# Optimization experiments

Hardware: AMD Instinct MI355X
Metric: run time of the kernel (lower is better)

## Reference

```python
import jax, jax.numpy as jnp
import numpy as np

N = 2048  # number of graph nodes


def setup_inputs() -> dict:
    key = jax.random.key(0)
    k1, k2, k3, k4 = jax.random.split(key, 4)
    # dense non-negative adjacency / association matrix
    A = jax.random.uniform(k1, (N, N), dtype=jnp.float32)
    # GTConv weights: layer0.conv1, layer0.conv2, layer1.conv1 (each (2,1,1,1))
    w1a = jax.random.normal(k2, (2, 1, 1, 1), dtype=jnp.float32)
    w1b = jax.random.normal(k3, (2, 1, 1, 1), dtype=jnp.float32)
    w2a = jax.random.normal(k4, (2, 1, 1, 1), dtype=jnp.float32)
    return {"A": A, "w1a": w1a, "w1b": w1b, "w2a": w2a}


def _gtconv(A4, w):
    # A4: (1,1,n,n); w: (2,1,1,1). softmax over dim=1 (singleton -> ones),
    # broadcast-multiply -> (2,1,n,n), sum over dim 0 -> (1,n,n)
    sw = jax.nn.softmax(w, axis=1)
    return jnp.sum(A4 * sw, axis=0)


def _norm(H):
    # H: (n,n). H <- diag(deg)^-1 @ (H + I), expressed as a row-scale
    # (identical math to the diagonal mm in the original).
    n = H.shape[0]
    H = H + jnp.eye(n, dtype=H.dtype)
    deg = jnp.sum(H, axis=1)
    deg = jnp.where(deg <= 1e-10, jnp.ones_like(deg), deg)
    return H / deg[:, None]


def reference(A, w1a, w1b, w2a):
    A4 = A[None, None]  # (1,1,n,n) after the forward's unsqueeze + broadcast
    # layer 0 (first=True)
    a = _gtconv(A4, w1a)            # (1,n,n)
    b = _gtconv(A4, w1b)            # (1,n,n)
    H = jnp.matmul(a, b)            # (1,n,n)
    # layer 1 (first=False): normalization of H[0], then bmm with conv(A)
    H_ = _norm(H[0])[None]          # (1,n,n)
    a2 = _gtconv(A4, w2a)           # (1,n,n)
    H2 = jnp.matmul(H_, a2)         # (1,n,n)
    return H2
```

## Files before the change

### kernel.cpp

```cpp
#include <hip/hip_runtime.h>
#include <stdint.h>

#define N 2048
#define TILE 128
#define BK 64
#define KH 16
#define LDSW 72
#define RSTR 17
#define NN ((size_t)N * (size_t)N)

typedef unsigned short u16;
typedef __bf16 bf16x8 __attribute__((ext_vector_type(8)));
typedef unsigned short ushortx8 __attribute__((ext_vector_type(8)));
typedef float floatx4 __attribute__((ext_vector_type(4)));

static __device__ __forceinline__ u16 f2bf(float f) {
  unsigned int u = __builtin_bit_cast(unsigned int, f);
  return (u16)((u + 0x7fffu + ((u >> 16) & 1u)) >> 16);
}
static __device__ __forceinline__ float bf2f(u16 h) {
  unsigned int u = ((unsigned int)h) << 16;
  return __builtin_bit_cast(float, u);
}

__global__ void cast_tr(const float* __restrict__ A, u16* __restrict__ Ab,
                        u16* __restrict__ Abt) {
  __shared__ float tile[32][33];
  const int tx = threadIdx.x, ty = threadIdx.y;
  const int c = blockIdx.x * 32 + tx;
#pragma unroll
  for (int i = 0; i < 4; i++) {
    const int r = blockIdx.y * 32 + ty + i * 8;
    const float v = A[(size_t)r * N + c];
    Ab[(size_t)r * N + c] = f2bf(v);
    tile[ty + i * 8][tx] = v;
  }
  __syncthreads();
  const int r2 = blockIdx.y * 32 + tx;
#pragma unroll
  for (int i = 0; i < 4; i++) {
    const int c2 = blockIdx.x * 32 + ty + i * 8;
    Abt[(size_t)c2 * N + r2] = f2bf(tile[tx][ty + i * 8]);
  }
}

__device__ __forceinline__ void gemm_core(const u16* __restrict__ L,
                                          const u16* __restrict__ Rt,
                                          float res[4][4]) {
  __shared__ __align__(16) u16 As[2][2][TILE * LDSW];
  __shared__ __align__(16) u16 Bs[2][2][TILE * LDSW];

  const int t = threadIdx.x;
  const int h = t >> 9;
  const int tl = t & 511;
  const int row0 = blockIdx.y * TILE;
  const int col0 = blockIdx.x * TILE;

  const int srow = tl >> 2;
  const int sc = (tl & 3) * 16;
  const u16* gA = L + (size_t)(row0 + srow) * N + h * (KH * BK) + sc;
  const u16* gB = Rt + (size_t)(col0 + srow) * N + h * (KH * BK) + sc;
  const int woff = srow * LDSW + sc;

  const int lane = t & 63;
  const int w = t >> 6;
  const int sub = w & 7;
  const int wr = (sub >> 2) * 64;
  const int wc = (sub & 3) * 32;
  const int lr = lane & 15;
  const int q = lane >> 4;
  const int abase = (wr + lr) * LDSW + q * 8;
  const int bbase = (wc + lr) * LDSW + q * 8;

  floatx4 acc[4][2];
#pragma unroll
  for (int i = 0; i < 4; i++)
#pragma unroll
    for (int j = 0; j < 2; j++) acc[i][j] = (floatx4){0.f, 0.f, 0.f, 0.f};

  ushortx8 sA[2][2], sB[2][2];
  sA[0][0] = *(const ushortx8*)(gA);
  sA[0][1] = *(const ushortx8*)(gA + 8);
  sB[0][0] = *(const ushortx8*)(gB);
  sB[0][1] = *(const ushortx8*)(gB + 8);
  sA[1][0] = *(const ushortx8*)(gA + BK);
  sA[1][1] = *(const ushortx8*)(gA + BK + 8);
  sB[1][0] = *(const ushortx8*)(gB + BK);
  sB[1][1] = *(const ushortx8*)(gB + BK + 8);
  *(ushortx8*)&As[h][0][woff] = sA[0][0];
  *(ushortx8*)&As[h][0][woff + 8] = sA[0][1];
  *(ushortx8*)&Bs[h][0][woff] = sB[0][0];
  *(ushortx8*)&Bs[h][0][woff + 8] = sB[0][1];
  __syncthreads();

#define GSTEP(i, cur, nxt)                                                    \
  {                                                                           \
    if ((i) + 2 < KH) {                                                       \
      sA[cur][0] = *(const ushortx8*)(gA + ((i) + 2) * BK);                   \
      sA[cur][1] = *(const ushortx8*)(gA + ((i) + 2) * BK + 8);               \
      sB[cur][0] = *(const ushortx8*)(gB + ((i) + 2) * BK);                   \
      sB[cur][1] = *(const ushortx8*)(gB + ((i) + 2) * BK + 8);               \
    }                                                                         \
    _Pragma("unroll") for (int kk = 0; kk < 2; kk++) {                        \
      bf16x8 af[4], bfr[2];                                                   \
      _Pragma("unroll") for (int mt = 0; mt < 4; mt++) af[mt] =               \
          __builtin_bit_cast(bf16x8,                                          \
              *(const ushortx8*)&As[h][cur][abase + kk * 32 + mt * 16 * LDSW]); \
      _Pragma("unroll") for (int nt = 0; nt < 2; nt++) bfr[nt] =              \
          __builtin_bit_cast(bf16x8,                                          \
              *(const ushortx8*)&Bs[h][cur][bbase + kk * 32 + nt * 16 * LDSW]); \
      _Pragma("unroll") for (int mt = 0; mt < 4; mt++)                        \
          _Pragma("unroll") for (int nt = 0; nt < 2; nt++) acc[mt][nt] =      \
              __builtin_amdgcn_mfma_f32_16x16x32_bf16(af[mt], bfr[nt],        \
                                                      acc[mt][nt], 0, 0, 0);  \
    }                                                                         \
    if ((i) + 1 < KH) {                                                       \
      *(ushortx8*)&As[h][nxt][woff] = sA[nxt][0];                             \
      *(ushortx8*)&As[h][nxt][woff + 8] = sA[nxt][1];                         \
      *(ushortx8*)&Bs[h][nxt][woff] = sB[nxt][0];                             \
      *(ushortx8*)&Bs[h][nxt][woff + 8] = sB[nxt][1];                         \
    }                                                                         \
    __syncthreads();                                                          \
  }

  for (int io = 0; io < KH; io += 2) {
    GSTEP(io, 0, 1)
    GSTEP(io + 1, 1, 0)
  }
#undef GSTEP

  float* red = (float*)&As[0][0][0];
  const int oh = 1 - h;
  const int rship = (sub * 2 + oh) * (64 * RSTR);
  const int rkeep = (sub * 2 + h) * (64 * RSTR);
#pragma unroll
  for (int mt = 0; mt < 4; mt++)
#pragma unroll
    for (int r = 0; r < 4; r++) {
      const float vship = h ? acc[mt][0][r] : acc[mt][1][r];
      red[rship + (mt * 16 + q * 4 + r) * RSTR + lr] = vship;
    }
  __syncthreads();
#pragma unroll
  for (int mt = 0; mt < 4; mt++)
#pragma unroll
    for (int r = 0; r < 4; r++) {
      const float vkeep = h ? acc[mt][1][r] : acc[mt][0][r];
      res[mt][r] = vkeep + red[rkeep + (mt * 16 + q * 4 + r) * RSTR + lr];
    }
}

__global__ __launch_bounds__(1024, 4) void gemm_aa(const u16* __restrict__ Ab,
                                                   const u16* __restrict__ Abt,
                                                   u16* __restrict__ Mb) {
  float res[4][4];
  gemm_core(Ab, Abt, res);
  const int t = threadIdx.x;
  const int lane = t & 63, w = t >> 6;
  const int sub = w & 7, h = w >> 3;
  const int wr = (sub >> 2) * 64, wc = (sub & 3) * 32;
  const int lr = lane & 15, q = lane >> 4;
  const int row0 = blockIdx.y * TILE, col0 = blockIdx.x * TILE;
  const int cc = col0 + wc + h * 16 + lr;
#pragma unroll
  for (int mt = 0; mt < 4; mt++)
#pragma unroll
    for (int r = 0; r < 4; r++) {
      const int rr = row0 + wr + mt * 16 + q * 4 + r;
      Mb[(size_t)rr * N + cc] = f2bf(res[mt][r]);
    }
}

__global__ void rowsum_k(const u16* __restrict__ Mb, float* __restrict__ rdeg) {
  const int row = blockIdx.x;
  const int t = threadIdx.x;
  const ushortx8 v = *((const ushortx8*)(Mb + (size_t)row * N) + t);
  float s = 0.f;
#pragma unroll
  for (int j = 0; j < 8; j++) s += bf2f(v[j]);
#pragma unroll
  for (int off = 32; off > 0; off >>= 1) s += __shfl_down(s, off, 64);
  __shared__ float ws[4];
  if ((t & 63) == 0) ws[t >> 6] = s;
  __syncthreads();
  if (t == 0) {
    float d = 4.f * (ws[0] + ws[1] + ws[2] + ws[3]) + 1.f;
    if (d <= 1e-10f) d = 1.f;
    rdeg[row] = 1.f / d;
  }
}

__global__ __launch_bounds__(1024, 4) void gemm_ma(const u16* __restrict__ Mb,
                                                   const u16* __restrict__ Abt,
                                                   const float* __restrict__ A,
                                                   const float* __restrict__ rdeg,
                                                   float* __restrict__ out) {
  float res[4][4];
  gemm_core(Mb, Abt, res);
  const int t = threadIdx.x;
  const int lane = t & 63, w = t >> 6;
  const int sub = w & 7, h = w >> 3;
  const int wr = (sub >> 2) * 64, wc = (sub & 3) * 32;
  const int lr = lane & 15, q = lane >> 4;
  const int row0 = blockIdx.y * TILE, col0 = blockIdx.x * TILE;
  const int cc = col0 + wc + h * 16 + lr;
#pragma unroll
  for (int mt = 0; mt < 4; mt++)
#pragma unroll
    for (int r = 0; r < 4; r++) {
      const int rr = row0 + wr + mt * 16 + q * 4 + r;
      out[(size_t)rr * N + cc] =
          (8.f * res[mt][r] + 2.f * A[(size_t)rr * N + cc]) * rdeg[rr];
    }
}

extern "C" void kernel_launch(void* const* d_in, const int* in_sizes, int n_in,
                              void* d_out, int out_size, void* d_ws, size_t ws_size,
                              hipStream_t stream) {
  const float* A = (const float*)d_in[0];
  float* out = (float*)d_out;
  char* ws = (char*)d_ws;
  u16* Ab = (u16*)ws;
  u16* Abt = (u16*)(ws + NN * 2);
  u16* Mb = (u16*)(ws + NN * 4);
  float* rdeg = (float*)(ws + NN * 6);

  cast_tr<<<dim3(N / 32, N / 32), dim3(32, 8), 0, stream>>>(A, Ab, Abt);
  gemm_aa<<<dim3(N / TILE, N / TILE), 1024, 0, stream>>>(Ab, Abt, Mb);
  rowsum_k<<<N, 256, 0, stream>>>(Mb, rdeg);
  gemm_ma<<<dim3(N / TILE, N / TILE), 1024, 0, stream>>>(Mb, Abt, A, rdeg, out);
}
```

Before: 128.6 us.

## Fuse row-degree sum into first GEMM epilogue and enlarge per-warp tiles

Removes the separate rowsum kernel by having gemm_aa accumulate fp32 row sums with shuffles and atomicAdd into a zeroed buffer, which gemm_ma then converts to the reciprocal degree. The GEMM core moves from 1024 to 512 threads, with each warp computing a 64x64 sub-tile and staging loads with single-step register prefetch instead of two steps ahead. This saves a launch and a full read of M, but adds atomics and more registers per thread. It also reduces prefetch depth, and the row sums now come from fp32 values rather than rounded bf16.

```diff
diff --git a/kernel.cpp b/kernel.cpp
--- a/kernel.cpp
+++ b/kernel.cpp
@@ -6,7 +6,7 @@
 #define BK 64
 #define KH 16
 #define LDSW 72
-#define RSTR 17
+#define RSTR 33
 #define NN ((size_t)N * (size_t)N)
 
 typedef unsigned short u16;
@@ -18,15 +18,15 @@
   unsigned int u = __builtin_bit_cast(unsigned int, f);
   return (u16)((u + 0x7fffu + ((u >> 16) & 1u)) >> 16);
 }
-static __device__ __forceinline__ float bf2f(u16 h) {
-  unsigned int u = ((unsigned int)h) << 16;
-  return __builtin_bit_cast(float, u);
-}
 
 __global__ void cast_tr(const float* __restrict__ A, u16* __restrict__ Ab,
-                        u16* __restrict__ Abt) {
+                        u16* __restrict__ Abt, float* __restrict__ rsum) {
   __shared__ float tile[32][33];
   const int tx = threadIdx.x, ty = threadIdx.y;
+  if (blockIdx.x == 0 && blockIdx.y == 0) {
+    const int tid = ty * 32 + tx;
+    for (int k = tid; k < N; k += 256) rsum[k] = 0.f;
+  }
   const int c = blockIdx.x * 32 + tx;
 #pragma unroll
   for (int i = 0; i < 4; i++) {
@@ -46,79 +46,85 @@
 
 __device__ __forceinline__ void gemm_core(const u16* __restrict__ L,
                                           const u16* __restrict__ Rt,
-                                          float res[4][4]) {
+                                          float res[4][8]) {
   __shared__ __align__(16) u16 As[2][2][TILE * LDSW];
   __shared__ __align__(16) u16 Bs[2][2][TILE * LDSW];
 
   const int t = threadIdx.x;
-  const int h = t >> 9;
-  const int tl = t & 511;
+  const int h = t >> 8;
+  const int tl = t & 255;
   const int row0 = blockIdx.y * TILE;
   const int col0 = blockIdx.x * TILE;
 
-  const int srow = tl >> 2;
-  const int sc = (tl & 3) * 16;
-  const u16* gA = L + (size_t)(row0 + srow) * N + h * (KH * BK) + sc;
-  const u16* gB = Rt + (size_t)(col0 + srow) * N + h * (KH * BK) + sc;
-  const int woff = srow * LDSW + sc;
+  int goff[4], woff[4];
+#pragma unroll
+  for (int c = 0; c < 4; c++) {
+    const int rowc = c * 32 + (tl >> 3);
+    const int colc = (tl & 7) * 8;
+    goff[c] = rowc * N + colc;
+    woff[c] = rowc * LDSW + colc;
+  }
+  const u16* gA = L + (size_t)row0 * N + h * (KH * BK);
+  const u16* gB = Rt + (size_t)col0 * N + h * (KH * BK);
 
   const int lane = t & 63;
   const int w = t >> 6;
-  const int sub = w & 7;
-  const int wr = (sub >> 2) * 64;
-  const int wc = (sub & 3) * 32;
+  const int sub = w & 3;
+  const int wr = (sub >> 1) * 64;
+  const int wc = (sub & 1) * 64;
   const int lr = lane & 15;
   const int q = lane >> 4;
   const int abase = (wr + lr) * LDSW + q * 8;
   const int bbase = (wc + lr) * LDSW + q * 8;
 
-  floatx4 acc[4][2];
+  floatx4 acc[4][4];
 #pragma unroll
   for (int i = 0; i < 4; i++)
 #pragma unroll
-    for (int j = 0; j < 2; j++) acc[i][j] = (floatx4){0.f, 0.f, 0.f, 0.f};
-
-  ushortx8 sA[2][2], sB[2][2];
-  sA[0][0] = *(const ushortx8*)(gA);
-  sA[0][1] = *(const ushortx8*)(gA + 8);
-  sB[0][0] = *(const ushortx8*)(gB);
-  sB[0][1] = *(const ushortx8*)(gB + 8);
-  sA[1][0] = *(const ushortx8*)(gA + BK);
-  sA[1][1] = *(const ushortx8*)(gA + BK + 8);
-  sB[1][0] = *(const ushortx8*)(gB + BK);
-  sB[1][1] = *(const ushortx8*)(gB + BK + 8);
-  *(ushortx8*)&As[h][0][woff] = sA[0][0];
-  *(ushortx8*)&As[h][0][woff + 8] = sA[0][1];
-  *(ushortx8*)&Bs[h][0][woff] = sB[0][0];
-  *(ushortx8*)&Bs[h][0][woff + 8] = sB[0][1];
+    for (int j = 0; j < 4; j++) acc[i][j] = (floatx4){0.f, 0.f, 0.f, 0.f};
+
+  {
+    ushortx8 pa[4], pb[4];
+#pragma unroll
+    for (int c = 0; c < 4; c++) {
+      pa[c] = *(const ushortx8*)(gA + goff[c]);
+      pb[c] = *(const ushortx8*)(gB + goff[c]);
+    }
+#pragma unroll
+    for (int c = 0; c < 4; c++) {
+      *(ushortx8*)&As[h][0][woff[c]] = pa[c];
+      *(ushortx8*)&Bs[h][0][woff[c]] = pb[c];
+    }
+  }
   __syncthreads();
 
 #define GSTEP(i, cur, nxt)                                                    \
   {                                                                           \
-    if ((i) + 2 < KH) {                                                       \
-      sA[cur][0] = *(const ushortx8*)(gA + ((i) + 2) * BK);                   \
-      sA[cur][1] = *(const ushortx8*)(gA + ((i) + 2) * BK + 8);               \
-      sB[cur][0] = *(const ushortx8*)(gB + ((i) + 2) * BK);                   \
-      sB[cur][1] = *(const ushortx8*)(gB + ((i) + 2) * BK + 8);               \
+    ushortx8 pa[4], pb[4];                                                    \
+    if ((i) + 1 < KH) {                                                       \
+      _Pragma("unroll") for (int c = 0; c < 4; c++) {                         \
+        pa[c] = *(const ushortx8*)(gA + goff[c] + ((i) + 1) * BK);            \
+        pb[c] = *(const ushortx8*)(gB + goff[c] + ((i) + 1) * BK);            \
+      }                                                                       \
     }                                                                         \
     _Pragma("unroll") for (int kk = 0; kk < 2; kk++) {                        \
-      bf16x8 af[4], bfr[2];                                                   \
+      bf16x8 af[4], bf[4];                                                    \
       _Pragma("unroll") for (int mt = 0; mt < 4; mt++) af[mt] =               \
           __builtin_bit_cast(bf16x8,                                          \
               *(const ushortx8*)&As[h][cur][abase + kk * 32 + mt * 16 * LDSW]); \
-      _Pragma("unroll") for (int nt = 0; nt < 2; nt++) bfr[nt] =              \
+      _Pragma("unroll") for (int nt = 0; nt < 4; nt++) bf[nt] =               \
           __builtin_bit_cast(bf16x8,                                          \
               *(const ushortx8*)&Bs[h][cur][bbase + kk * 32 + nt * 16 * LDSW]); \
       _Pragma("unroll") for (int mt = 0; mt < 4; mt++)                        \
-          _Pragma("unroll") for (int nt = 0; nt < 2; nt++) acc[mt][nt] =      \
-              __builtin_amdgcn_mfma_f32_16x16x32_bf16(af[mt], bfr[nt],        \
+          _Pragma("unroll") for (int nt = 0; nt < 4; nt++) acc[mt][nt] =      \
+              __builtin_amdgcn_mfma_f32_16x16x32_bf16(af[mt], bf[nt],         \
                                                       acc[mt][nt], 0, 0, 0);  \
     }                                                                         \
     if ((i) + 1 < KH) {                                                       \
-      *(ushortx8*)&As[h][nxt][woff] = sA[nxt][0];                             \
-      *(ushortx8*)&As[h][nxt][woff + 8] = sA[nxt][1];                         \
-      *(ushortx8*)&Bs[h][nxt][woff] = sB[nxt][0];                             \
-      *(ushortx8*)&Bs[h][nxt][woff + 8] = sB[nxt][1];                         \
+      _Pragma("unroll") for (int c = 0; c < 4; c++) {                         \
+        *(ushortx8*)&As[h][nxt][woff[c]] = pa[c];                             \
+        *(ushortx8*)&Bs[h][nxt][woff[c]] = pb[c];                             \
+      }                                                                       \
     }                                                                         \
     __syncthreads();                                                          \
   }
@@ -136,81 +142,85 @@
 #pragma unroll
   for (int mt = 0; mt < 4; mt++)
 #pragma unroll
-    for (int r = 0; r < 4; r++) {
-      const float vship = h ? acc[mt][0][r] : acc[mt][1][r];
-      red[rship + (mt * 16 + q * 4 + r) * RSTR + lr] = vship;
-    }
+    for (int j = 0; j < 2; j++)
+#pragma unroll
+      for (int r = 0; r < 4; r++) {
+        const float vship = h ? acc[mt][j][r] : acc[mt][j + 2][r];
+        red[rship + (mt * 16 + q * 4 + r) * RSTR + j * 16 + lr] = vship;
+      }
   __syncthreads();
 #pragma unroll
   for (int mt = 0; mt < 4; mt++)
 #pragma unroll
-    for (int r = 0; r < 4; r++) {
-      const float vkeep = h ? acc[mt][1][r] : acc[mt][0][r];
-      res[mt][r] = vkeep + red[rkeep + (mt * 16 + q * 4 + r) * RSTR + lr];
-    }
-}
-
-__global__ __launch_bounds__(1024, 4) void gemm_aa(const u16* __restrict__ Ab,
-                                                   const u16* __restrict__ Abt,
-                                                   u16* __restrict__ Mb) {
-  float res[4][4];
+    for (int j = 0; j < 2; j++)
+#pragma unroll
+      for (int r = 0; r < 4; r++) {
+        const float vkeep = h ? acc[mt][j + 2][r] : acc[mt][j][r];
+        res[mt][j * 4 + r] =
+            vkeep + red[rkeep + (mt * 16 + q * 4 + r) * RSTR + j * 16 + lr];
+      }
+}
+
+__global__ __launch_bounds__(512, 2) void gemm_aa(const u16* __restrict__ Ab,
+                                                  const u16* __restrict__ Abt,
+                                                  u16* __restrict__ Mb,
+                                                  float* __restrict__ rsum) {
+  float res[4][8];
   gemm_core(Ab, Abt, res);
   const int t = threadIdx.x;
   const int lane = t & 63, w = t >> 6;
-  const int sub = w & 7, h = w >> 3;
-  const int wr = (sub >> 2) * 64, wc = (sub & 3) * 32;
+  const int sub = w & 3, h = w >> 2;
+  const int wr = (sub >> 1) * 64, wc = (sub & 1) * 64;
   const int lr = lane & 15, q = lane >> 4;
   const int row0 = blockIdx.y * TILE, col0 = blockIdx.x * TILE;
-  const int cc = col0 + wc + h * 16 + lr;
 #pragma unroll
   for (int mt = 0; mt < 4; mt++)
 #pragma unroll
     for (int r = 0; r < 4; r++) {
       const int rr = row0 + wr + mt * 16 + q * 4 + r;
-      Mb[(size_t)rr * N + cc] = f2bf(res[mt][r]);
-    }
-}
-
-__global__ void rowsum_k(const u16* __restrict__ Mb, float* __restrict__ rdeg) {
-  const int row = blockIdx.x;
-  const int t = threadIdx.x;
-  const ushortx8 v = *((const ushortx8*)(Mb + (size_t)row * N) + t);
-  float s = 0.f;
-#pragma unroll
-  for (int j = 0; j < 8; j++) s += bf2f(v[j]);
-#pragma unroll
-  for (int off = 32; off > 0; off >>= 1) s += __shfl_down(s, off, 64);
-  __shared__ float ws[4];
-  if ((t & 63) == 0) ws[t >> 6] = s;
-  __syncthreads();
-  if (t == 0) {
-    float d = 4.f * (ws[0] + ws[1] + ws[2] + ws[3]) + 1.f;
-    if (d <= 1e-10f) d = 1.f;
-    rdeg[row] = 1.f / d;
-  }
-}
-
-__global__ __launch_bounds__(1024, 4) void gemm_ma(const u16* __restrict__ Mb,
-                                                   const u16* __restrict__ Abt,
-                                                   const float* __restrict__ A,
-                                                   const float* __restrict__ rdeg,
-                                                   float* __restrict__ out) {
-  float res[4][4];
+      float s = 0.f;
+#pragma unroll
+      for (int j = 0; j < 2; j++) {
+        const float v = res[mt][j * 4 + r];
+        s += v;
+        const int cc = col0 + wc + (h * 2 + j) * 16 + lr;
+        Mb[(size_t)rr * N + cc] = f2bf(v);
+      }
+      s += __shfl_xor(s, 1, 64);
+      s += __shfl_xor(s, 2, 64);
+      s += __shfl_xor(s, 4, 64);
+      s += __shfl_xor(s, 8, 64);
+      if (lr == 0) atomicAdd(&rsum[rr], s);
+    }
+}
+
+__global__ __launch_bounds__(512, 2) void gemm_ma(const u16* __restrict__ Mb,
+                                                  const u16* __restrict__ Abt,
+                                                  const float* __restrict__ A,
+                                                  const float* __restrict__ rsum,
+                                                  float* __restrict__ out) {
+  float res[4][8];
   gemm_core(Mb, Abt, res);
   const int t = threadIdx.x;
   const int lane = t & 63, w = t >> 6;
-  const int sub = w & 7, h = w >> 3;
-  const int wr = (sub >> 2) * 64, wc = (sub & 3) * 32;
+  const int sub = w & 3, h = w >> 2;
+  const int wr = (sub >> 1) * 64, wc = (sub & 1) * 64;
   const int lr = lane & 15, q = lane >> 4;
   const int row0 = blockIdx.y * TILE, col0 = blockIdx.x * TILE;
-  const int cc = col0 + wc + h * 16 + lr;
 #pragma unroll
   for (int mt = 0; mt < 4; mt++)
 #pragma unroll
     for (int r = 0; r < 4; r++) {
       const int rr = row0 + wr + mt * 16 + q * 4 + r;
-      out[(size_t)rr * N + cc] =
-          (8.f * res[mt][r] + 2.f * A[(size_t)rr * N + cc]) * rdeg[rr];
+      float d = 4.f * rsum[rr] + 1.f;
+      if (d <= 1e-10f) d = 1.f;
+      const float rd = 1.f / d;
+#pragma unroll
+      for (int j = 0; j < 2; j++) {
+        const int cc = col0 + wc + (h * 2 + j) * 16 + lr;
+        out[(size_t)rr * N + cc] =
+            (8.f * res[mt][j * 4 + r] + 2.f * A[(size_t)rr * N + cc]) * rd;
+      }
     }
 }
 
@@ -223,10 +233,9 @@
   u16* Ab = (u16*)ws;
   u16* Abt = (u16*)(ws + NN * 2);
   u16* Mb = (u16*)(ws + NN * 4);
-  float* rdeg = (float*)(ws + NN * 6);
-
-  cast_tr<<<dim3(N / 32, N / 32), dim3(32, 8), 0, stream>>>(A, Ab, Abt);
-  gemm_aa<<<dim3(N / TILE, N / TILE), 1024, 0, stream>>>(Ab, Abt, Mb);
-  rowsum_k<<<N, 256, 0, stream>>>(Mb, rdeg);
-  gemm_ma<<<dim3(N / TILE, N / TILE), 1024, 0, stream>>>(Mb, Abt, A, rdeg, out);
-}
+  float* rsum = (float*)(ws + NN * 6);
+
+  cast_tr<<<dim3(N / 32, N / 32), dim3(32, 8), 0, stream>>>(A, Ab, Abt, rsum);
+  gemm_aa<<<dim3(N / TILE, N / TILE), 512, 0, stream>>>(Ab, Abt, Mb, rsum);
+  gemm_ma<<<dim3(N / TILE, N / TILE), 512, 0, stream>>>(Mb, Abt, A, rsum, out);
+}
```

Result: slower. 136.8 us (+6.4%).

## Fuse row-degree reduction into first GEMM epilogue via atomics; raise MFMA priority

Applied to the files above, without the earlier changes.

Removes the separate rowsum kernel: the first GEMM's epilogue reduces each row's partial sums across lanes with shuffles and atomically adds them into a global row-sum buffer. The buffer is zeroed inside the cast kernel. The second GEMM now computes the degree and divides per element. It also brackets the MFMA block with s_setprio to favour the matrix instructions. This saves a kernel launch and a reread of Mb, at the cost of float atomics (non-deterministic summation order) and a reduction on fp32 values rather than the rounded bf16 ones.

```diff
diff --git a/kernel.cpp b/kernel.cpp
--- a/kernel.cpp
+++ b/kernel.cpp
@@ -18,15 +18,15 @@
   unsigned int u = __builtin_bit_cast(unsigned int, f);
   return (u16)((u + 0x7fffu + ((u >> 16) & 1u)) >> 16);
 }
-static __device__ __forceinline__ float bf2f(u16 h) {
-  unsigned int u = ((unsigned int)h) << 16;
-  return __builtin_bit_cast(float, u);
-}
 
 __global__ void cast_tr(const float* __restrict__ A, u16* __restrict__ Ab,
-                        u16* __restrict__ Abt) {
+                        u16* __restrict__ Abt, float* __restrict__ rsum) {
   __shared__ float tile[32][33];
   const int tx = threadIdx.x, ty = threadIdx.y;
+  if (blockIdx.x == 0 && blockIdx.y == 0) {
+    const int tid = ty * 32 + tx;
+    for (int k = tid; k < N; k += 256) rsum[k] = 0.f;
+  }
   const int c = blockIdx.x * 32 + tx;
 #pragma unroll
   for (int i = 0; i < 4; i++) {
@@ -109,10 +109,12 @@
       _Pragma("unroll") for (int nt = 0; nt < 2; nt++) bfr[nt] =              \
           __builtin_bit_cast(bf16x8,                                          \
               *(const ushortx8*)&Bs[h][cur][bbase + kk * 32 + nt * 16 * LDSW]); \
+      __builtin_amdgcn_s_setprio(1);                                          \
       _Pragma("unroll") for (int mt = 0; mt < 4; mt++)                        \
           _Pragma("unroll") for (int nt = 0; nt < 2; nt++) acc[mt][nt] =      \
               __builtin_amdgcn_mfma_f32_16x16x32_bf16(af[mt], bfr[nt],        \
                                                       acc[mt][nt], 0, 0, 0);  \
+      __builtin_amdgcn_s_setprio(0);                                          \
     }                                                                         \
     if ((i) + 1 < KH) {                                                       \
       *(ushortx8*)&As[h][nxt][woff] = sA[nxt][0];                             \
@@ -152,7 +154,8 @@
 
 __global__ __launch_bounds__(1024, 4) void gemm_aa(const u16* __restrict__ Ab,
                                                    const u16* __restrict__ Abt,
-                                                   u16* __restrict__ Mb) {
+                                                   u16* __restrict__ Mb,
+                                                   float* __restrict__ rsum) {
   float res[4][4];
   gemm_core(Ab, Abt, res);
   const int t = threadIdx.x;
@@ -167,33 +170,21 @@
 #pragma unroll
     for (int r = 0; r < 4; r++) {
       const int rr = row0 + wr + mt * 16 + q * 4 + r;
-      Mb[(size_t)rr * N + cc] = f2bf(res[mt][r]);
-    }
-}
-
-__global__ void rowsum_k(const u16* __restrict__ Mb, float* __restrict__ rdeg) {
-  const int row = blockIdx.x;
-  const int t = threadIdx.x;
-  const ushortx8 v = *((const ushortx8*)(Mb + (size_t)row * N) + t);
-  float s = 0.f;
-#pragma unroll
-  for (int j = 0; j < 8; j++) s += bf2f(v[j]);
-#pragma unroll
-  for (int off = 32; off > 0; off >>= 1) s += __shfl_down(s, off, 64);
-  __shared__ float ws[4];
-  if ((t & 63) == 0) ws[t >> 6] = s;
-  __syncthreads();
-  if (t == 0) {
-    float d = 4.f * (ws[0] + ws[1] + ws[2] + ws[3]) + 1.f;
-    if (d <= 1e-10f) d = 1.f;
-    rdeg[row] = 1.f / d;
-  }
+      const float v = res[mt][r];
+      Mb[(size_t)rr * N + cc] = f2bf(v);
+      float s = v;
+      s += __shfl_xor(s, 1, 64);
+      s += __shfl_xor(s, 2, 64);
+      s += __shfl_xor(s, 4, 64);
+      s += __shfl_xor(s, 8, 64);
+      if (lr == 0) atomicAdd(&rsum[rr], s);
+    }
 }
 
 __global__ __launch_bounds__(1024, 4) void gemm_ma(const u16* __restrict__ Mb,
                                                    const u16* __restrict__ Abt,
                                                    const float* __restrict__ A,
-                                                   const float* __restrict__ rdeg,
+                                                   const float* __restrict__ rsum,
                                                    float* __restrict__ out) {
   float res[4][4];
   gemm_core(Mb, Abt, res);
@@ -209,8 +200,10 @@
 #pragma unroll
     for (int r = 0; r < 4; r++) {
       const int rr = row0 + wr + mt * 16 + q * 4 + r;
+      float d = 4.f * rsum[rr] + 1.f;
+      if (d <= 1e-10f) d = 1.f;
       out[(size_t)rr * N + cc] =
-          (8.f * res[mt][r] + 2.f * A[(size_t)rr * N + cc]) * rdeg[rr];
+          (8.f * res[mt][r] + 2.f * A[(size_t)rr * N + cc]) / d;
     }
 }
 
@@ -223,10 +216,9 @@
   u16* Ab = (u16*)ws;
   u16* Abt = (u16*)(ws + NN * 2);
   u16* Mb = (u16*)(ws + NN * 4);
-  float* rdeg = (float*)(ws + NN * 6);
-
-  cast_tr<<<dim3(N / 32, N / 32), dim3(32, 8), 0, stream>>>(A, Ab, Abt);
-  gemm_aa<<<dim3(N / TILE, N / TILE), 1024, 0, stream>>>(Ab, Abt, Mb);
-  rowsum_k<<<N, 256, 0, stream>>>(Mb, rdeg);
-  gemm_ma<<<dim3(N / TILE, N / TILE), 1024, 0, stream>>>(Mb, Abt, A, rdeg, out);
-}
+  float* rsum = (float*)(ws + NN * 6);
+
+  cast_tr<<<dim3(N / 32, N / 32), dim3(32, 8), 0, stream>>>(A, Ab, Abt, rsum);
+  gemm_aa<<<dim3(N / TILE, N / TILE), 1024, 0, stream>>>(Ab, Abt, Mb, rsum);
+  gemm_ma<<<dim3(N / TILE, N / TILE), 1024, 0, stream>>>(Mb, Abt, A, rsum, out);
+}
```

After: 144.0 us. 1.12x slower.

## Load GEMM tiles directly into LDS with XOR-swizzled unpadded layout

Applied to the files above, without the earlier changes.

Replaces the register-staged global-to-LDS copies in the shared GEMM core with global_load_lds direct transfers, and drops the padded LDS row stride in favour of an XOR swizzle on 16-byte chunks to avoid bank conflicts. The prefetch distance shrinks from two stages held in registers to one stage written straight into the alternate LDS buffer. This is meant to cut VGPR use and the extra LDS store instructions. The cost is a shorter load-ahead window and reliance on the hardware direct-to-LDS path being correctly ordered by the existing barriers.

```diff
diff --git a/kernel.cpp b/kernel.cpp
--- a/kernel.cpp
+++ b/kernel.cpp
@@ -5,8 +5,7 @@
 #define TILE 128
 #define BK 64
 #define KH 16
-#define LDSW 72
-#define RSTR 17
+#define RSTR 16
 #define NN ((size_t)N * (size_t)N)
 
 typedef unsigned short u16;
@@ -21,6 +20,12 @@
 static __device__ __forceinline__ float bf2f(u16 h) {
   unsigned int u = ((unsigned int)h) << 16;
   return __builtin_bit_cast(float, u);
+}
+
+static __device__ __forceinline__ void gload16(const u16* g, u16* l) {
+  __builtin_amdgcn_global_load_lds(
+      (const __attribute__((address_space(1))) void*)g,
+      (__attribute__((address_space(3))) void*)l, 16, 0, 0);
 }
 
 __global__ void cast_tr(const float* __restrict__ A, u16* __restrict__ Ab,
@@ -46,31 +51,34 @@
 
 __device__ __forceinline__ void gemm_core(const u16* __restrict__ L,
                                           const u16* __restrict__ Rt,
+                                          int row0, int col0,
                                           float res[4][4]) {
-  __shared__ __align__(16) u16 As[2][2][TILE * LDSW];
-  __shared__ __align__(16) u16 Bs[2][2][TILE * LDSW];
-
-  const int t = threadIdx.x;
-  const int h = t >> 9;
-  const int tl = t & 511;
-  const int row0 = blockIdx.y * TILE;
-  const int col0 = blockIdx.x * TILE;
-
-  const int srow = tl >> 2;
-  const int sc = (tl & 3) * 16;
-  const u16* gA = L + (size_t)(row0 + srow) * N + h * (KH * BK) + sc;
-  const u16* gB = Rt + (size_t)(col0 + srow) * N + h * (KH * BK) + sc;
-  const int woff = srow * LDSW + sc;
-
+  __shared__ __align__(16) u16 As[2][2][TILE * BK];
+  __shared__ __align__(16) u16 Bs[2][2][TILE * BK];
+
+  const int t = threadIdx.x;
   const int lane = t & 63;
   const int w = t >> 6;
-  const int sub = w & 7;
+  const int h = w >> 3;
+  const int wv = w & 7;
+
+  const int rl = lane >> 3;
+  const int cl = ((lane & 7) ^ rl) * 8;
+  const int g0 = wv * 2;
+  const u16* gA0 = L + (size_t)(row0 + g0 * 8 + rl) * N + h * (KH * BK) + cl;
+  const u16* gA1 = gA0 + 8 * N;
+  const u16* gB0 = Rt + (size_t)(col0 + g0 * 8 + rl) * N + h * (KH * BK) + cl;
+  const u16* gB1 = gB0 + 8 * N;
+  const int ld0 = g0 * 512;
+
+  const int sub = wv;
   const int wr = (sub >> 2) * 64;
   const int wc = (sub & 3) * 32;
   const int lr = lane & 15;
   const int q = lane >> 4;
-  const int abase = (wr + lr) * LDSW + q * 8;
-  const int bbase = (wc + lr) * LDSW + q * 8;
+  const int lx = lr & 7;
+  const int arow = (wr + lr) * BK;
+  const int brow = (wc + lr) * BK;
 
   floatx4 acc[4][2];
 #pragma unroll
@@ -78,48 +86,35 @@
 #pragma unroll
     for (int j = 0; j < 2; j++) acc[i][j] = (floatx4){0.f, 0.f, 0.f, 0.f};
 
-  ushortx8 sA[2][2], sB[2][2];
-  sA[0][0] = *(const ushortx8*)(gA);
-  sA[0][1] = *(const ushortx8*)(gA + 8);
-  sB[0][0] = *(const ushortx8*)(gB);
-  sB[0][1] = *(const ushortx8*)(gB + 8);
-  sA[1][0] = *(const ushortx8*)(gA + BK);
-  sA[1][1] = *(const ushortx8*)(gA + BK + 8);
-  sB[1][0] = *(const ushortx8*)(gB + BK);
-  sB[1][1] = *(const ushortx8*)(gB + BK + 8);
-  *(ushortx8*)&As[h][0][woff] = sA[0][0];
-  *(ushortx8*)&As[h][0][woff + 8] = sA[0][1];
-  *(ushortx8*)&Bs[h][0][woff] = sB[0][0];
-  *(ushortx8*)&Bs[h][0][woff + 8] = sB[0][1];
+  gload16(gA0, &As[h][0][ld0]);
+  gload16(gA1, &As[h][0][ld0 + 512]);
+  gload16(gB0, &Bs[h][0][ld0]);
+  gload16(gB1, &Bs[h][0][ld0 + 512]);
   __syncthreads();
 
 #define GSTEP(i, cur, nxt)                                                    \
   {                                                                           \
-    if ((i) + 2 < KH) {                                                       \
-      sA[cur][0] = *(const ushortx8*)(gA + ((i) + 2) * BK);                   \
-      sA[cur][1] = *(const ushortx8*)(gA + ((i) + 2) * BK + 8);               \
-      sB[cur][0] = *(const ushortx8*)(gB + ((i) + 2) * BK);                   \
-      sB[cur][1] = *(const ushortx8*)(gB + ((i) + 2) * BK + 8);               \
+    if ((i) + 1 < KH) {                                                       \
+      gload16(gA0 + ((i) + 1) * BK, &As[h][nxt][ld0]);                        \
+      gload16(gA1 + ((i) + 1) * BK, &As[h][nxt][ld0 + 512]);                  \
+      gload16(gB0 + ((i) + 1) * BK, &Bs[h][nxt][ld0]);                        \
+      gload16(gB1 + ((i) + 1) * BK, &Bs[h][nxt][ld0 + 512]);                  \
     }                                                                         \
     _Pragma("unroll") for (int kk = 0; kk < 2; kk++) {                        \
       bf16x8 af[4], bfr[2];                                                   \
       _Pragma("unroll") for (int mt = 0; mt < 4; mt++) af[mt] =               \
-          __builtin_bit_cast(bf16x8,                                          \
-              *(const ushortx8*)&As[h][cur][abase + kk * 32 + mt * 16 * LDSW]); \
+          __builtin_bit_cast(                                                 \
+              bf16x8, *(const ushortx8*)&As[h][cur][arow + mt * 16 * BK +     \
+                                                    ((kk * 4 + q) ^ lx) * 8]); \
       _Pragma("unroll") for (int nt = 0; nt < 2; nt++) bfr[nt] =              \
-          __builtin_bit_cast(bf16x8,                                          \
-              *(const ushortx8*)&Bs[h][cur][bbase + kk * 32 + nt * 16 * LDSW]); \
+          __builtin_bit_cast(                                                 \
+              bf16x8, *(const ushortx8*)&Bs[h][cur][brow + nt * 16 * BK +     \
+                                                    ((kk * 4 + q) ^ lx) * 8]); \
       _Pragma("unroll") for (int mt = 0; mt < 4; mt++)                        \
           _Pragma("unroll") for (int nt = 0; nt < 2; nt++) acc[mt][nt] =      \
               __builtin_amdgcn_mfma_f32_16x16x32_bf16(af[mt], bfr[nt],        \
                                                       acc[mt][nt], 0, 0, 0);  \
     }                                                                         \
-    if ((i) + 1 < KH) {                                                       \
-      *(ushortx8*)&As[h][nxt][woff] = sA[nxt][0];                             \
-      *(ushortx8*)&As[h][nxt][woff + 8] = sA[nxt][1];                         \
-      *(ushortx8*)&Bs[h][nxt][woff] = sB[nxt][0];                             \
-      *(ushortx8*)&Bs[h][nxt][woff + 8] = sB[nxt][1];                         \
-    }                                                                         \
     __syncthreads();                                                          \
   }
 
@@ -153,14 +148,14 @@
 __global__ __launch_bounds__(1024, 4) void gemm_aa(const u16* __restrict__ Ab,
                                                    const u16* __restrict__ Abt,
                                                    u16* __restrict__ Mb) {
+  const int row0 = blockIdx.y * TILE, col0 = blockIdx.x * TILE;
   float res[4][4];
-  gemm_core(Ab, Abt, res);
+  gemm_core(Ab, Abt, row0, col0, res);
   const int t = threadIdx.x;
   const int lane = t & 63, w = t >> 6;
   const int sub = w & 7, h = w >> 3;
   const int wr = (sub >> 2) * 64, wc = (sub & 3) * 32;
   const int lr = lane & 15, q = lane >> 4;
-  const int row0 = blockIdx.y * TILE, col0 = blockIdx.x * TILE;
   const int cc = col0 + wc + h * 16 + lr;
 #pragma unroll
   for (int mt = 0; mt < 4; mt++)
@@ -195,14 +190,14 @@
                                                    const float* __restrict__ A,
                                                    const float* __restrict__ rdeg,
                                                    float* __restrict__ out) {
+  const int row0 = blockIdx.y * TILE, col0 = blockIdx.x * TILE;
   float res[4][4];
-  gemm_core(Mb, Abt, res);
+  gemm_core(Mb, Abt, row0, col0, res);
   const int t = threadIdx.x;
   const int lane = t & 63, w = t >> 6;
   const int sub = w & 7, h = w >> 3;
   const int wr = (sub >> 2) * 64, wc = (sub & 3) * 32;
   const int lr = lane & 15, q = lane >> 4;
-  const int row0 = blockIdx.y * TILE, col0 = blockIdx.x * TILE;
   const int cc = col0 + wc + h * 16 + lr;
 #pragma unroll
   for (int mt = 0; mt < 4; mt++)
```

Result: slower. 135.2 us (+5.1%).
